# Performance work log

Hardware: AMD Instinct MI355X
Metric: run time of the kernel (lower is better)

Reference implementation:

```python
import jax, jax.numpy as jnp
import numpy as np

E, H, I, G, T, TOPK = 8, 2048, 5632, 128, 256, 2
FP8_MAX = 448.0


def setup_inputs() -> dict:
    key = jax.random.key(0)
    ks = jax.random.split(key, 8)
    hidden_states = jax.random.normal(ks[0], (T, H), jnp.float32)
    router_logits = jax.random.normal(ks[1], (T, E), jnp.float32)
    # unpacked INT4 values in [-8, 7], stored as int8 (modeling unpack_int4->int8)
    w3w1_q = jax.random.randint(ks[2], (E, H, 2 * I), -8, 8, dtype=jnp.int32).astype(jnp.int8)
    w2_q = jax.random.randint(ks[3], (E, I, H), -8, 8, dtype=jnp.int32).astype(jnp.int8)
    # group-wise weight scales: [in_dim/G, out_dim] per expert
    w3w1_scale = jax.random.uniform(ks[4], (E, H // G, 2 * I), jnp.float32, 0.005, 0.02)
    w2_scale = jax.random.uniform(ks[5], (E, I // G, H), jnp.float32, 0.005, 0.02)
    # per-expert static activation scales (p3_p1 = max(p1,p3) pre-folded)
    input_scale_fc1 = jax.random.uniform(ks[6], (E,), jnp.float32, 0.5, 1.5)
    input_scale_fc2 = jax.random.uniform(ks[7], (E,), jnp.float32, 0.5, 1.5)
    return dict(hidden_states=hidden_states, router_logits=router_logits,
                w3w1_q=w3w1_q, w2_q=w2_q, w3w1_scale=w3w1_scale, w2_scale=w2_scale,
                input_scale_fc1=input_scale_fc1, input_scale_fc2=input_scale_fc2)


def _fp8_qdq(x, s):
    # quantize activation to fp8_e4m3 (clamp + round-to-fp8) then dequantize
    q = jnp.clip(x / s, -FP8_MAX, FP8_MAX).astype(jnp.float8_e4m3fn)
    return q.astype(jnp.float32)


def _dequant(w_q, w_scale):
    # w_q: [in, out] int8; w_scale: [in/G, out] -> repeat each group G rows
    return w_q.astype(jnp.float32) * jnp.repeat(w_scale, G, axis=0)


def _routing(router_logits):
    probs = jax.nn.softmax(router_logits, axis=-1)            # [T, E]
    vals, idx = jax.lax.top_k(probs, TOPK)                    # [T, K]
    scales = vals / jnp.sum(vals, axis=-1, keepdims=True)     # renormalize
    # per-token gate weight for every expert, zero if not selected: [T, E]
    gate = jnp.sum(jax.nn.one_hot(idx, E, dtype=scales.dtype) * scales[..., None], axis=1)
    return gate


def reference(hidden_states, router_logits, w3w1_q, w2_q, w3w1_scale, w2_scale,
              input_scale_fc1, input_scale_fc2):
    gate = _routing(router_logits)                            # [T, E]
    out = jnp.zeros_like(hidden_states)
    for e in range(E):  # fixed small expert loop (structurally distinct weights)
        s1 = input_scale_fc1[e]
        act = _fp8_qdq(hidden_states, s1)                     # [T, H]
        w_fc1 = _dequant(w3w1_q[e], w3w1_scale[e])            # [H, 2I]
        fc1 = (act @ w_fc1) * s1                              # [T, 2I]
        up, gt = fc1[:, :I], fc1[:, I:]                       # chunk: (w3 | w1)
        h = up * jax.nn.silu(gt)                              # [T, I]
        s2 = input_scale_fc2[e]
        act2 = _fp8_qdq(h, s2)
        w_fc2 = _dequant(w2_q[e], w2_scale[e])                # [I, H]
        fc2 = (act2 @ w_fc2) * s2                             # [T, H]
        out = out + fc2 * gate[:, e:e + 1]
    return out
```

## Files before the change

kernel.cpp:

```cpp
#include <hip/hip_runtime.h>
#include <hip/hip_bf16.h>
#include <hip/hip_fp8.h>
#include <cstdint>
#include <cstddef>

#define E_ 8
#define H_ 2048
#define I_ 5632
#define N1_ (2 * I_)
#define G_ 128
#define T_ 256
#define RPE 256
#define SLOTS (E_ * RPE)

typedef __attribute__((ext_vector_type(4))) float f32x4;
typedef __attribute__((ext_vector_type(8))) __bf16 bf16x8;

#define WS_CNT 0
#define WS_TOKEN 64
#define WS_GATE (64 + SLOTS * 4)
#define WS_A1 32768
#define WS_A2 (WS_A1 + SLOTS * H_ * 2)

__device__ __forceinline__ uint32_t pack_bf16x2(float a, float b) {
  union { float f; uint32_t u; } ua, ub;
  ua.f = a; ub.f = b;
  uint32_t ra = (ua.u + 0x7FFFu + ((ua.u >> 16) & 1u)) >> 16;
  uint32_t rb = (ub.u + 0x7FFFu + ((ub.u >> 16) & 1u)) & 0xFFFF0000u;
  return ra | rb;
}

__device__ __forceinline__ float fp8_qdq1(float x) {
  x = fminf(fmaxf(x, -448.0f), 448.0f);
  __hip_fp8_e4m3 q(x);
  return (float)q;
}

__global__ void routing_kernel(const float* __restrict__ logits,
                               int* __restrict__ cnt,
                               int* __restrict__ token_of, float* __restrict__ gate_of) {
  __shared__ int s_cnt[E_];
  int t = threadIdx.x;
  if (t < E_) s_cnt[t] = 0;
  __syncthreads();
  float l[E_];
#pragma unroll
  for (int e = 0; e < E_; e++) l[e] = logits[t * E_ + e];
  int i0 = 0;
#pragma unroll
  for (int e = 1; e < E_; e++) if (l[e] > l[i0]) i0 = e;
  int i1 = (i0 == 0) ? 1 : 0;
#pragma unroll
  for (int e = 0; e < E_; e++) if (e != i0 && l[e] > l[i1]) i1 = e;
  float g0 = 1.0f / (1.0f + expf(l[i1] - l[i0]));
  float g1 = 1.0f - g0;
  int s0 = atomicAdd(&s_cnt[i0], 1);
  int s1 = atomicAdd(&s_cnt[i1], 1);
  token_of[i0 * RPE + s0] = t;  gate_of[i0 * RPE + s0] = g0;
  token_of[i1 * RPE + s1] = t;  gate_of[i1 * RPE + s1] = g1;
  __syncthreads();
  if (t < E_) cnt[t] = s_cnt[t];
  for (int idx = t; idx < SLOTS; idx += 256) {
    int e = idx >> 8, r = idx & (RPE - 1);
    if (r >= s_cnt[e]) { token_of[idx] = 0; gate_of[idx] = 0.0f; }
  }
}

__global__ void gather_kernel(const float* __restrict__ hidden,
                              const float* __restrict__ is1,
                              const int* __restrict__ cnt,
                              const int* __restrict__ token_of,
                              __hip_bfloat16* __restrict__ A1) {
  int sg = blockIdx.x;
  int e = sg >> 8, r = sg & (RPE - 1);
  bool pad = (r >= cnt[e]);
  uint4 u;
  if (pad) {
    u.x = u.y = u.z = u.w = 0u;
  } else {
    int t = token_of[sg];
    float s1 = is1[e];
    const float4* hp = (const float4*)(hidden + (size_t)t * H_ + threadIdx.x * 8);
    float4 x0 = hp[0], x1 = hp[1];
    float q0 = fp8_qdq1(x0.x / s1), q1 = fp8_qdq1(x0.y / s1);
    float q2 = fp8_qdq1(x0.z / s1), q3 = fp8_qdq1(x0.w / s1);
    float q4 = fp8_qdq1(x1.x / s1), q5 = fp8_qdq1(x1.y / s1);
    float q6 = fp8_qdq1(x1.z / s1), q7 = fp8_qdq1(x1.w / s1);
    u.x = pack_bf16x2(q0, q1); u.y = pack_bf16x2(q2, q3);
    u.z = pack_bf16x2(q4, q5); u.w = pack_bf16x2(q6, q7);
  }
  ((uint4*)(A1 + (size_t)sg * H_))[threadIdx.x] = u;
}

__global__ __launch_bounds__(256) void fc1_kernel(
    const int* __restrict__ w1, const float* __restrict__ w1s,
    const float* __restrict__ is1v, const float* __restrict__ is2v,
    const __hip_bfloat16* __restrict__ A1, __hip_bfloat16* __restrict__ A2) {
  __shared__ __hip_bfloat16 Bt[2][4][64][8];
  const int e = blockIdx.y;
  const int j0 = blockIdx.x * 32;
  const int tid = threadIdx.x;
  const int wave = tid >> 6, lane = tid & 63;
  const int lm = lane & 15, kq = lane >> 4;
  const int sn = lane;
  const int kb4 = wave * 4;
  const int gcol = (sn < 32) ? (j0 + sn) : (I_ + j0 + (sn - 32));
  const int* wp = w1 + (size_t)e * H_ * N1_ + gcol;
  const float* sbase = w1s + (size_t)e * (H_ / G_) * N1_ + gcol;
  const __hip_bfloat16* abase = A1 + (size_t)e * RPE * H_;

  f32x4 acc[4][4];
#pragma unroll
  for (int a = 0; a < 4; a++)
#pragma unroll
    for (int b = 0; b < 4; b++) acc[a][b] = (f32x4){0.f, 0.f, 0.f, 0.f};

  int wA[8], wB[8];
  float scA = sbase[0], scB = scA;
#pragma unroll
  for (int g = 0; g < 2; g++)
#pragma unroll
    for (int c = 0; c < 4; c++)
      wA[g * 4 + c] = __builtin_nontemporal_load(wp + (size_t)(kb4 + 16 * g + c) * N1_);
#pragma unroll
  for (int g = 0; g < 2; g++) {
    uint32_t p0 = pack_bf16x2((float)wA[g * 4 + 0] * scA, (float)wA[g * 4 + 1] * scA);
    uint32_t p1 = pack_bf16x2((float)wA[g * 4 + 2] * scA, (float)wA[g * 4 + 3] * scA);
    *(uint2*)&Bt[0][(wave >> 1) + 2 * g][sn][(wave & 1) * 4] = make_uint2(p0, p1);
  }
  wp += (size_t)32 * N1_;
#pragma unroll
  for (int g = 0; g < 2; g++)
#pragma unroll
    for (int c = 0; c < 4; c++)
      wB[g * 4 + c] = __builtin_nontemporal_load(wp + (size_t)(kb4 + 16 * g + c) * N1_);
  wp += (size_t)32 * N1_;

  const __hip_bfloat16* aptr[4];
#pragma unroll
  for (int mj = 0; mj < 4; mj++)
    aptr[mj] = abase + (size_t)((wave * 4 + mj) * 16 + lm) * H_ + kq * 8;
  uint4 afr[4];
#pragma unroll
  for (int mj = 0; mj < 4; mj++) afr[mj] = *(const uint4*)aptr[mj];

  __syncthreads();

  for (int ks = 0; ks < 64; ks++) {
    const int buf = ks & 1;
    int wC[8]; float scC = scB;
    if (ks + 2 < 64) {
      if (((ks + 2) & 3) == 0) scC = sbase[(size_t)((ks + 2) >> 2) * N1_];
#pragma unroll
      for (int g = 0; g < 2; g++)
#pragma unroll
        for (int c = 0; c < 4; c++)
          wC[g * 4 + c] = __builtin_nontemporal_load(wp + (size_t)(kb4 + 16 * g + c) * N1_);
    }
    uint4 anx[4];
    if (ks + 1 < 64) {
#pragma unroll
      for (int mj = 0; mj < 4; mj++)
        anx[mj] = *(const uint4*)(aptr[mj] + (ks + 1) * 32);
    }
#pragma unroll
    for (int f = 0; f < 4; f++) {
      union { uint4 u; bf16x8 v; } bu;
      bu.u = *(const uint4*)&Bt[buf][kq][f * 16 + lm][0];
#pragma unroll
      for (int mj = 0; mj < 4; mj++) {
        union { uint4 u; bf16x8 v; } au;
        au.u = afr[mj];
        acc[mj][f] = __builtin_amdgcn_mfma_f32_16x16x32_bf16(au.v, bu.v, acc[mj][f], 0, 0, 0);
      }
    }
    if (ks + 1 < 64) {
#pragma unroll
      for (int g = 0; g < 2; g++) {
        uint32_t p0 = pack_bf16x2((float)wB[g * 4 + 0] * scB, (float)wB[g * 4 + 1] * scB);
        uint32_t p1 = pack_bf16x2((float)wB[g * 4 + 2] * scB, (float)wB[g * 4 + 3] * scB);
        *(uint2*)&Bt[buf ^ 1][(wave >> 1) + 2 * g][sn][(wave & 1) * 4] = make_uint2(p0, p1);
      }
    }
    __syncthreads();
#pragma unroll
    for (int i = 0; i < 8; i++) wB[i] = wC[i];
    scB = scC;
#pragma unroll
    for (int mj = 0; mj < 4; mj++) afr[mj] = anx[mj];
    wp += (size_t)32 * N1_;
  }

  const float s1 = is1v[e], s2 = is2v[e];
  __hip_bfloat16* a2base = A2 + (size_t)(e * RPE) * I_ + j0;
#pragma unroll
  for (int mj = 0; mj < 4; mj++) {
    int mrow = (wave * 4 + mj) * 16 + kq * 4;
#pragma unroll
    for (int r = 0; r < 4; r++) {
#pragma unroll
      for (int f = 0; f < 2; f++) {
        float up = acc[mj][f][r] * s1;
        float gt = acc[mj][f + 2][r] * s1;
        float h = up * (gt / (1.0f + expf(-gt)));
        float q = fp8_qdq1(h / s2);
        a2base[(size_t)(mrow + r) * I_ + f * 16 + lm] = __float2bfloat16(q);
      }
    }
  }
}

__global__ __launch_bounds__(256) void fc2_kernel(
    const int* __restrict__ w2, const float* __restrict__ w2s,
    const float* __restrict__ is2v, const int* __restrict__ cnt,
    const int* __restrict__ token_of, const float* __restrict__ gate_of,
    const __hip_bfloat16* __restrict__ A2, float* __restrict__ out) {
  __shared__ __hip_bfloat16 Bt[2][4][64][8];
  const int e = blockIdx.y;
  const int n0 = blockIdx.x * 64;
  const int z = blockIdx.z;
  const int tid = threadIdx.x;
  const int wave = tid >> 6, lane = tid & 63;
  const int lm = lane & 15, kq = lane >> 4;
  const int sn = lane;
  const int kb4 = wave * 4;
  const int gcol = n0 + sn;
  const int* wp = w2 + (size_t)e * I_ * H_ + (size_t)(z * 44 * 32) * H_ + gcol;
  const float* sbase = w2s + (size_t)e * (I_ / G_) * H_ + gcol;
  const __hip_bfloat16* abase = A2 + (size_t)e * RPE * I_;

  f32x4 acc[4][4];
#pragma unroll
  for (int a = 0; a < 4; a++)
#pragma unroll
    for (int b = 0; b < 4; b++) acc[a][b] = (f32x4){0.f, 0.f, 0.f, 0.f};

  int wA[8], wB[8];
  float scA = sbase[(size_t)(z * 11) * H_], scB = scA;
#pragma unroll
  for (int g = 0; g < 2; g++)
#pragma unroll
    for (int c = 0; c < 4; c++)
      wA[g * 4 + c] = __builtin_nontemporal_load(wp + (size_t)(kb4 + 16 * g + c) * H_);
#pragma unroll
  for (int g = 0; g < 2; g++) {
    uint32_t p0 = pack_bf16x2((float)wA[g * 4 + 0] * scA, (float)wA[g * 4 + 1] * scA);
    uint32_t p1 = pack_bf16x2((float)wA[g * 4 + 2] * scA, (float)wA[g * 4 + 3] * scA);
    *(uint2*)&Bt[0][(wave >> 1) + 2 * g][sn][(wave & 1) * 4] = make_uint2(p0, p1);
  }
  wp += (size_t)32 * H_;
#pragma unroll
  for (int g = 0; g < 2; g++)
#pragma unroll
    for (int c = 0; c < 4; c++)
      wB[g * 4 + c] = __builtin_nontemporal_load(wp + (size_t)(kb4 + 16 * g + c) * H_);
  wp += (size_t)32 * H_;

  const __hip_bfloat16* aptr[4];
#pragma unroll
  for (int mj = 0; mj < 4; mj++)
    aptr[mj] = abase + (size_t)((wave * 4 + mj) * 16 + lm) * I_ + (size_t)z * 44 * 32 + kq * 8;
  uint4 afr[4];
#pragma unroll
  for (int mj = 0; mj < 4; mj++) afr[mj] = *(const uint4*)aptr[mj];

  __syncthreads();

  for (int ks = 0; ks < 44; ks++) {
    const int buf = ks & 1;
    int wC[8]; float scC = scB;
    if (ks + 2 < 44) {
      if (((ks + 2) & 3) == 0) scC = sbase[(size_t)(z * 11 + ((ks + 2) >> 2)) * H_];
#pragma unroll
      for (int g = 0; g < 2; g++)
#pragma unroll
        for (int c = 0; c < 4; c++)
          wC[g * 4 + c] = __builtin_nontemporal_load(wp + (size_t)(kb4 + 16 * g + c) * H_);
    }
    uint4 anx[4];
    if (ks + 1 < 44) {
#pragma unroll
      for (int mj = 0; mj < 4; mj++)
        anx[mj] = *(const uint4*)(aptr[mj] + (ks + 1) * 32);
    }
#pragma unroll
    for (int f = 0; f < 4; f++) {
      union { uint4 u; bf16x8 v; } bu;
      bu.u = *(const uint4*)&Bt[buf][kq][f * 16 + lm][0];
#pragma unroll
      for (int mj = 0; mj < 4; mj++) {
        union { uint4 u; bf16x8 v; } au;
        au.u = afr[mj];
        acc[mj][f] = __builtin_amdgcn_mfma_f32_16x16x32_bf16(au.v, bu.v, acc[mj][f], 0, 0, 0);
      }
    }
    if (ks + 1 < 44) {
#pragma unroll
      for (int g = 0; g < 2; g++) {
        uint32_t p0 = pack_bf16x2((float)wB[g * 4 + 0] * scB, (float)wB[g * 4 + 1] * scB);
        uint32_t p1 = pack_bf16x2((float)wB[g * 4 + 2] * scB, (float)wB[g * 4 + 3] * scB);
        *(uint2*)&Bt[buf ^ 1][(wave >> 1) + 2 * g][sn][(wave & 1) * 4] = make_uint2(p0, p1);
      }
    }
    __syncthreads();
#pragma unroll
    for (int i = 0; i < 8; i++) wB[i] = wC[i];
    scB = scC;
#pragma unroll
    for (int mj = 0; mj < 4; mj++) afr[mj] = anx[mj];
    wp += (size_t)32 * H_;
  }

  const float s2 = is2v[e];
  const int c_n = cnt[e];
#pragma unroll
  for (int mj = 0; mj < 4; mj++) {
    int sl0 = (wave * 4 + mj) * 16 + kq * 4;
#pragma unroll
    for (int r = 0; r < 4; r++) {
      int slot = sl0 + r;
      if (slot < c_n) {
        int t = token_of[e * RPE + slot];
        float gv = gate_of[e * RPE + slot] * s2;
#pragma unroll
        for (int f = 0; f < 4; f++)
          atomicAdd(out + (size_t)t * H_ + n0 + f * 16 + lm, acc[mj][f][r] * gv);
      }
    }
  }
}

extern "C" void kernel_launch(void* const* d_in, const int* in_sizes, int n_in,
                              void* d_out, int out_size, void* d_ws, size_t ws_size,
                              hipStream_t stream) {
  const float* hidden = (const float*)d_in[0];
  const float* logits = (const float*)d_in[1];
  const int* w1 = (const int*)d_in[2];
  const int* w2 = (const int*)d_in[3];
  const float* w1s = (const float*)d_in[4];
  const float* w2s = (const float*)d_in[5];
  const float* is1 = (const float*)d_in[6];
  const float* is2 = (const float*)d_in[7];
  float* out = (float*)d_out;
  char* ws = (char*)d_ws;
  int* cnt = (int*)(ws + WS_CNT);
  int* token_of = (int*)(ws + WS_TOKEN);
  float* gate_of = (float*)(ws + WS_GATE);
  __hip_bfloat16* A1 = (__hip_bfloat16*)(ws + WS_A1);
  __hip_bfloat16* A2 = (__hip_bfloat16*)(ws + WS_A2);

  hipMemsetAsync(d_out, 0, (size_t)T_ * H_ * sizeof(float), stream);
  routing_kernel<<<1, 256, 0, stream>>>(logits, cnt, token_of, gate_of);
  gather_kernel<<<SLOTS, 256, 0, stream>>>(hidden, is1, cnt, token_of, A1);
  fc1_kernel<<<dim3(I_ / 32, E_), 256, 0, stream>>>(w1, w1s, is1, is2, A1, A2);
  fc2_kernel<<<dim3(H_ / 64, E_, 4), 256, 0, stream>>>(w2, w2s, is2, cnt, token_of,
                                                       gate_of, A2, out);
}
```

Before: 1.379 ms.

## Skip MFMA work on empty expert row tiles and use non-draining barriers

Reads each expert's routed-token count in the fc1 and fc2 kernels and computes how many 16-row tiles per wave hold real tokens. Loads, MFMAs and epilogue stores are skipped for inactive tiles, and tiles are interleaved across waves (mj*4+wave) so the active work is spread evenly. The __syncthreads calls are replaced by a barrier that waits only on LDS counters, so outstanding global weight prefetches are not drained each step. The kernels remain bound by streaming the weights, so skipping compute may help little, and the custom barrier relies on the in-flight global loads never being needed before their own wait.

```diff
diff --git a/kernel.cpp b/kernel.cpp
--- a/kernel.cpp
+++ b/kernel.cpp
@@ -34,6 +34,13 @@
   x = fminf(fmaxf(x, -448.0f), 448.0f);
   __hip_fp8_e4m3 q(x);
   return (float)q;
+}
+
+__device__ __forceinline__ void block_sync_nodrain() {
+  __builtin_amdgcn_sched_barrier(0);
+  asm volatile("s_waitcnt lgkmcnt(0)" ::: "memory");
+  __builtin_amdgcn_s_barrier();
+  __builtin_amdgcn_sched_barrier(0);
 }
 
 __global__ void routing_kernel(const float* __restrict__ logits,
@@ -95,6 +102,7 @@
 __global__ __launch_bounds__(256) void fc1_kernel(
     const int* __restrict__ w1, const float* __restrict__ w1s,
     const float* __restrict__ is1v, const float* __restrict__ is2v,
+    const int* __restrict__ cnt,
     const __hip_bfloat16* __restrict__ A1, __hip_bfloat16* __restrict__ A2) {
   __shared__ __hip_bfloat16 Bt[2][4][64][8];
   const int e = blockIdx.y;
@@ -109,6 +117,10 @@
   const float* sbase = w1s + (size_t)e * (H_ / G_) * N1_ + gcol;
   const __hip_bfloat16* abase = A1 + (size_t)e * RPE * H_;
 
+  const int C16 = (cnt[e] + 15) >> 4;
+  int nact = (C16 - wave + 3) >> 2;
+  if (nact < 0) nact = 0;
+
   f32x4 acc[4][4];
 #pragma unroll
   for (int a = 0; a < 4; a++)
@@ -137,14 +149,14 @@
   wp += (size_t)32 * N1_;
 
   const __hip_bfloat16* aptr[4];
-#pragma unroll
-  for (int mj = 0; mj < 4; mj++)
-    aptr[mj] = abase + (size_t)((wave * 4 + mj) * 16 + lm) * H_ + kq * 8;
   uint4 afr[4];
 #pragma unroll
-  for (int mj = 0; mj < 4; mj++) afr[mj] = *(const uint4*)aptr[mj];
-
-  __syncthreads();
+  for (int mj = 0; mj < 4; mj++) {
+    aptr[mj] = abase + (size_t)((mj * 4 + wave) * 16 + lm) * H_ + kq * 8;
+    if (mj < nact) afr[mj] = *(const uint4*)aptr[mj];
+  }
+
+  block_sync_nodrain();
 
   for (int ks = 0; ks < 64; ks++) {
     const int buf = ks & 1;
@@ -161,17 +173,33 @@
     if (ks + 1 < 64) {
 #pragma unroll
       for (int mj = 0; mj < 4; mj++)
-        anx[mj] = *(const uint4*)(aptr[mj] + (ks + 1) * 32);
-    }
-#pragma unroll
-    for (int f = 0; f < 4; f++) {
-      union { uint4 u; bf16x8 v; } bu;
-      bu.u = *(const uint4*)&Bt[buf][kq][f * 16 + lm][0];
-#pragma unroll
-      for (int mj = 0; mj < 4; mj++) {
-        union { uint4 u; bf16x8 v; } au;
-        au.u = afr[mj];
-        acc[mj][f] = __builtin_amdgcn_mfma_f32_16x16x32_bf16(au.v, bu.v, acc[mj][f], 0, 0, 0);
+        if (mj < nact) anx[mj] = *(const uint4*)(aptr[mj] + (ks + 1) * 32);
+    }
+    if (nact == 4) {
+#pragma unroll
+      for (int f = 0; f < 4; f++) {
+        union { uint4 u; bf16x8 v; } bu;
+        bu.u = *(const uint4*)&Bt[buf][kq][f * 16 + lm][0];
+#pragma unroll
+        for (int mj = 0; mj < 4; mj++) {
+          union { uint4 u; bf16x8 v; } au;
+          au.u = afr[mj];
+          acc[mj][f] = __builtin_amdgcn_mfma_f32_16x16x32_bf16(au.v, bu.v, acc[mj][f], 0, 0, 0);
+        }
+      }
+    } else if (nact > 0) {
+#pragma unroll
+      for (int f = 0; f < 4; f++) {
+        union { uint4 u; bf16x8 v; } bu;
+        bu.u = *(const uint4*)&Bt[buf][kq][f * 16 + lm][0];
+#pragma unroll
+        for (int mj = 0; mj < 4; mj++) {
+          if (mj < nact) {
+            union { uint4 u; bf16x8 v; } au;
+            au.u = afr[mj];
+            acc[mj][f] = __builtin_amdgcn_mfma_f32_16x16x32_bf16(au.v, bu.v, acc[mj][f], 0, 0, 0);
+          }
+        }
       }
     }
     if (ks + 1 < 64) {
@@ -182,7 +210,7 @@
         *(uint2*)&Bt[buf ^ 1][(wave >> 1) + 2 * g][sn][(wave & 1) * 4] = make_uint2(p0, p1);
       }
     }
-    __syncthreads();
+    block_sync_nodrain();
 #pragma unroll
     for (int i = 0; i < 8; i++) wB[i] = wC[i];
     scB = scC;
@@ -195,16 +223,18 @@
   __hip_bfloat16* a2base = A2 + (size_t)(e * RPE) * I_ + j0;
 #pragma unroll
   for (int mj = 0; mj < 4; mj++) {
-    int mrow = (wave * 4 + mj) * 16 + kq * 4;
-#pragma unroll
-    for (int r = 0; r < 4; r++) {
-#pragma unroll
-      for (int f = 0; f < 2; f++) {
-        float up = acc[mj][f][r] * s1;
-        float gt = acc[mj][f + 2][r] * s1;
-        float h = up * (gt / (1.0f + expf(-gt)));
-        float q = fp8_qdq1(h / s2);
-        a2base[(size_t)(mrow + r) * I_ + f * 16 + lm] = __float2bfloat16(q);
+    if (mj < nact) {
+      int mrow = (mj * 4 + wave) * 16 + kq * 4;
+#pragma unroll
+      for (int r = 0; r < 4; r++) {
+#pragma unroll
+        for (int f = 0; f < 2; f++) {
+          float up = acc[mj][f][r] * s1;
+          float gt = acc[mj][f + 2][r] * s1;
+          float h = up * (gt / (1.0f + expf(-gt)));
+          float q = fp8_qdq1(h / s2);
+          a2base[(size_t)(mrow + r) * I_ + f * 16 + lm] = __float2bfloat16(q);
+        }
       }
     }
   }
@@ -229,6 +259,11 @@
   const float* sbase = w2s + (size_t)e * (I_ / G_) * H_ + gcol;
   const __hip_bfloat16* abase = A2 + (size_t)e * RPE * I_;
 
+  const int c_n = cnt[e];
+  const int C16 = (c_n + 15) >> 4;
+  int nact = (C16 - wave + 3) >> 2;
+  if (nact < 0) nact = 0;
+
   f32x4 acc[4][4];
 #pragma unroll
   for (int a = 0; a < 4; a++)
@@ -257,14 +292,14 @@
   wp += (size_t)32 * H_;
 
   const __hip_bfloat16* aptr[4];
-#pragma unroll
-  for (int mj = 0; mj < 4; mj++)
-    aptr[mj] = abase + (size_t)((wave * 4 + mj) * 16 + lm) * I_ + (size_t)z * 44 * 32 + kq * 8;
   uint4 afr[4];
 #pragma unroll
-  for (int mj = 0; mj < 4; mj++) afr[mj] = *(const uint4*)aptr[mj];
-
-  __syncthreads();
+  for (int mj = 0; mj < 4; mj++) {
+    aptr[mj] = abase + (size_t)((mj * 4 + wave) * 16 + lm) * I_ + (size_t)z * 44 * 32 + kq * 8;
+    if (mj < nact) afr[mj] = *(const uint4*)aptr[mj];
+  }
+
+  block_sync_nodrain();
 
   for (int ks = 0; ks < 44; ks++) {
     const int buf = ks & 1;
@@ -281,17 +316,33 @@
     if (ks + 1 < 44) {
 #pragma unroll
       for (int mj = 0; mj < 4; mj++)
-        anx[mj] = *(const uint4*)(aptr[mj] + (ks + 1) * 32);
-    }
-#pragma unroll
-    for (int f = 0; f < 4; f++) {
-      union { uint4 u; bf16x8 v; } bu;
-      bu.u = *(const uint4*)&Bt[buf][kq][f * 16 + lm][0];
-#pragma unroll
-      for (int mj = 0; mj < 4; mj++) {
-        union { uint4 u; bf16x8 v; } au;
-        au.u = afr[mj];
-        acc[mj][f] = __builtin_amdgcn_mfma_f32_16x16x32_bf16(au.v, bu.v, acc[mj][f], 0, 0, 0);
+        if (mj < nact) anx[mj] = *(const uint4*)(aptr[mj] + (ks + 1) * 32);
+    }
+    if (nact == 4) {
+#pragma unroll
+      for (int f = 0; f < 4; f++) {
+        union { uint4 u; bf16x8 v; } bu;
+        bu.u = *(const uint4*)&Bt[buf][kq][f * 16 + lm][0];
+#pragma unroll
+        for (int mj = 0; mj < 4; mj++) {
+          union { uint4 u; bf16x8 v; } au;
+          au.u = afr[mj];
+          acc[mj][f] = __builtin_amdgcn_mfma_f32_16x16x32_bf16(au.v, bu.v, acc[mj][f], 0, 0, 0);
+        }
+      }
+    } else if (nact > 0) {
+#pragma unroll
+      for (int f = 0; f < 4; f++) {
+        union { uint4 u; bf16x8 v; } bu;
+        bu.u = *(const uint4*)&Bt[buf][kq][f * 16 + lm][0];
+#pragma unroll
+        for (int mj = 0; mj < 4; mj++) {
+          if (mj < nact) {
+            union { uint4 u; bf16x8 v; } au;
+            au.u = afr[mj];
+            acc[mj][f] = __builtin_amdgcn_mfma_f32_16x16x32_bf16(au.v, bu.v, acc[mj][f], 0, 0, 0);
+          }
+        }
       }
     }
     if (ks + 1 < 44) {
@@ -302,7 +353,7 @@
         *(uint2*)&Bt[buf ^ 1][(wave >> 1) + 2 * g][sn][(wave & 1) * 4] = make_uint2(p0, p1);
       }
     }
-    __syncthreads();
+    block_sync_nodrain();
 #pragma unroll
     for (int i = 0; i < 8; i++) wB[i] = wC[i];
     scB = scC;
@@ -312,19 +363,20 @@
   }
 
   const float s2 = is2v[e];
-  const int c_n = cnt[e];
 #pragma unroll
   for (int mj = 0; mj < 4; mj++) {
-    int sl0 = (wave * 4 + mj) * 16 + kq * 4;
-#pragma unroll
-    for (int r = 0; r < 4; r++) {
-      int slot = sl0 + r;
-      if (slot < c_n) {
-        int t = token_of[e * RPE + slot];
-        float gv = gate_of[e * RPE + slot] * s2;
-#pragma unroll
-        for (int f = 0; f < 4; f++)
-          atomicAdd(out + (size_t)t * H_ + n0 + f * 16 + lm, acc[mj][f][r] * gv);
+    if (mj < nact) {
+      int sl0 = (mj * 4 + wave) * 16 + kq * 4;
+#pragma unroll
+      for (int r = 0; r < 4; r++) {
+        int slot = sl0 + r;
+        if (slot < c_n) {
+          int t = token_of[e * RPE + slot];
+          float gv = gate_of[e * RPE + slot] * s2;
+#pragma unroll
+          for (int f = 0; f < 4; f++)
+            atomicAdd(out + (size_t)t * H_ + n0 + f * 16 + lm, acc[mj][f][r] * gv);
+        }
       }
     }
   }
@@ -352,7 +404,7 @@
   hipMemsetAsync(d_out, 0, (size_t)T_ * H_ * sizeof(float), stream);
   routing_kernel<<<1, 256, 0, stream>>>(logits, cnt, token_of, gate_of);
   gather_kernel<<<SLOTS, 256, 0, stream>>>(hidden, is1, cnt, token_of, A1);
-  fc1_kernel<<<dim3(I_ / 32, E_), 256, 0, stream>>>(w1, w1s, is1, is2, A1, A2);
+  fc1_kernel<<<dim3(I_ / 32, E_), 256, 0, stream>>>(w1, w1s, is1, is2, cnt, A1, A2);
   fc2_kernel<<<dim3(H_ / 64, E_, 4), 256, 0, stream>>>(w2, w2s, is2, cnt, token_of,
                                                        gate_of, A2, out);
 }
```

After: 1.277 ms. 1.08x faster.

## Skip empty expert row tiles and restructure weight pipeline with non-draining barriers

Applied to the files above, without the earlier changes.

Both GEMM kernels now read each expert's token count and run MFMAs, A loads and epilogue stores only for the 16-row tiles that hold routed tokens. The row tiles are interleaved across waves so the active work is spread evenly. Weight loads become 2-wide int vector loads with per-pair scale loads, and the k loop is unrolled by two with explicit register double buffers. A custom barrier waits only on LDS counters, so in-flight global loads are not drained at each sync. This mainly cuts wasted MFMA work, since about 64 of 256 slots per expert are used on average, but it adds more manual scheduling and relies on the asm waitcnt being correct.

```diff
diff --git a/kernel.cpp b/kernel.cpp
--- a/kernel.cpp
+++ b/kernel.cpp
@@ -15,6 +15,7 @@
 
 typedef __attribute__((ext_vector_type(4))) float f32x4;
 typedef __attribute__((ext_vector_type(8))) __bf16 bf16x8;
+typedef __attribute__((ext_vector_type(2))) int i32x2;
 
 #define WS_CNT 0
 #define WS_TOKEN 64
@@ -34,6 +35,54 @@
   x = fminf(fmaxf(x, -448.0f), 448.0f);
   __hip_fp8_e4m3 q(x);
   return (float)q;
+}
+
+__device__ __forceinline__ void block_sync_nodrain() {
+  __builtin_amdgcn_sched_barrier(0);
+  asm volatile("s_waitcnt lgkmcnt(0)" ::: "memory");
+  __builtin_amdgcn_s_barrier();
+  __builtin_amdgcn_sched_barrier(0);
+}
+
+__device__ __forceinline__ void wissue(const int* __restrict__ wpt, size_t ldN, int m,
+                                       i32x2 wv[4]) {
+#pragma unroll
+  for (int c = 0; c < 4; ++c)
+    wv[c] = __builtin_nontemporal_load(
+        reinterpret_cast<const i32x2*>(wpt + ((size_t)m * 32 + c) * ldN));
+}
+
+__device__ __forceinline__ void wstage(__hip_bfloat16 (*Btb)[64][8], int kqw, int n0, int h4,
+                                       const i32x2 wv[4], float2 sc) {
+  uint32_t a0 = pack_bf16x2((float)wv[0].x * sc.x, (float)wv[1].x * sc.x);
+  uint32_t a1 = pack_bf16x2((float)wv[2].x * sc.x, (float)wv[3].x * sc.x);
+  uint32_t b0 = pack_bf16x2((float)wv[0].y * sc.y, (float)wv[1].y * sc.y);
+  uint32_t b1 = pack_bf16x2((float)wv[2].y * sc.y, (float)wv[3].y * sc.y);
+  *(uint2*)&Btb[kqw][n0][h4] = make_uint2(a0, a1);
+  *(uint2*)&Btb[kqw][n0 + 1][h4] = make_uint2(b0, b1);
+}
+
+__device__ __forceinline__ void aissue(const __hip_bfloat16* const aptr[4], int m, int nact,
+                                       uint4 av[4]) {
+#pragma unroll
+  for (int mj = 0; mj < 4; ++mj)
+    if (mj < nact) av[mj] = *(const uint4*)(aptr[mj] + (size_t)m * 32);
+}
+
+__device__ __forceinline__ void do_mfma(const __hip_bfloat16 (*Btb)[64][8], int kq, int lm,
+                                        int nact, const uint4 afr[4], f32x4 acc[4][4]) {
+#pragma unroll
+  for (int f = 0; f < 4; ++f) {
+    union { uint4 u; bf16x8 v; } bu;
+    bu.u = *(const uint4*)&Btb[kq][f * 16 + lm][0];
+#pragma unroll
+    for (int mj = 0; mj < 4; ++mj)
+      if (mj < nact) {
+        union { uint4 u; bf16x8 v; } au;
+        au.u = afr[mj];
+        acc[mj][f] = __builtin_amdgcn_mfma_f32_16x16x32_bf16(au.v, bu.v, acc[mj][f], 0, 0, 0);
+      }
+  }
 }
 
 __global__ void routing_kernel(const float* __restrict__ logits,
@@ -95,6 +144,7 @@
 __global__ __launch_bounds__(256) void fc1_kernel(
     const int* __restrict__ w1, const float* __restrict__ w1s,
     const float* __restrict__ is1v, const float* __restrict__ is2v,
+    const int* __restrict__ cnt,
     const __hip_bfloat16* __restrict__ A1, __hip_bfloat16* __restrict__ A2) {
   __shared__ __hip_bfloat16 Bt[2][4][64][8];
   const int e = blockIdx.y;
@@ -102,109 +152,76 @@
   const int tid = threadIdx.x;
   const int wave = tid >> 6, lane = tid & 63;
   const int lm = lane & 15, kq = lane >> 4;
-  const int sn = lane;
-  const int kb4 = wave * 4;
-  const int gcol = (sn < 32) ? (j0 + sn) : (I_ + j0 + (sn - 32));
-  const int* wp = w1 + (size_t)e * H_ * N1_ + gcol;
-  const float* sbase = w1s + (size_t)e * (H_ / G_) * N1_ + gcol;
+  const int np = tid & 31, kg = tid >> 5;
+  const int kqw = kg >> 1, h4 = (kg & 1) * 4;
+  const int n0s = np * 2;
+  const int gc2 = (n0s < 32) ? (j0 + n0s) : (I_ + j0 + (n0s - 32));
+  const int* wpt = w1 + (size_t)e * H_ * N1_ + (size_t)(kg * 4) * N1_ + gc2;
+  const float* spt = w1s + (size_t)e * (H_ / G_) * N1_ + gc2;
   const __hip_bfloat16* abase = A1 + (size_t)e * RPE * H_;
 
+  const int C16 = (cnt[e] + 15) >> 4;
+  int nact = (C16 - wave + 3) >> 2;
+  if (nact < 0) nact = 0;
+
   f32x4 acc[4][4];
 #pragma unroll
   for (int a = 0; a < 4; a++)
 #pragma unroll
     for (int b = 0; b < 4; b++) acc[a][b] = (f32x4){0.f, 0.f, 0.f, 0.f};
 
-  int wA[8], wB[8];
-  float scA = sbase[0], scB = scA;
-#pragma unroll
-  for (int g = 0; g < 2; g++)
-#pragma unroll
-    for (int c = 0; c < 4; c++)
-      wA[g * 4 + c] = __builtin_nontemporal_load(wp + (size_t)(kb4 + 16 * g + c) * N1_);
-#pragma unroll
-  for (int g = 0; g < 2; g++) {
-    uint32_t p0 = pack_bf16x2((float)wA[g * 4 + 0] * scA, (float)wA[g * 4 + 1] * scA);
-    uint32_t p1 = pack_bf16x2((float)wA[g * 4 + 2] * scA, (float)wA[g * 4 + 3] * scA);
-    *(uint2*)&Bt[0][(wave >> 1) + 2 * g][sn][(wave & 1) * 4] = make_uint2(p0, p1);
-  }
-  wp += (size_t)32 * N1_;
-#pragma unroll
-  for (int g = 0; g < 2; g++)
-#pragma unroll
-    for (int c = 0; c < 4; c++)
-      wB[g * 4 + c] = __builtin_nontemporal_load(wp + (size_t)(kb4 + 16 * g + c) * N1_);
-  wp += (size_t)32 * N1_;
-
   const __hip_bfloat16* aptr[4];
 #pragma unroll
   for (int mj = 0; mj < 4; mj++)
-    aptr[mj] = abase + (size_t)((wave * 4 + mj) * 16 + lm) * H_ + kq * 8;
-  uint4 afr[4];
-#pragma unroll
-  for (int mj = 0; mj < 4; mj++) afr[mj] = *(const uint4*)aptr[mj];
-
-  __syncthreads();
-
-  for (int ks = 0; ks < 64; ks++) {
-    const int buf = ks & 1;
-    int wC[8]; float scC = scB;
-    if (ks + 2 < 64) {
-      if (((ks + 2) & 3) == 0) scC = sbase[(size_t)((ks + 2) >> 2) * N1_];
-#pragma unroll
-      for (int g = 0; g < 2; g++)
-#pragma unroll
-        for (int c = 0; c < 4; c++)
-          wC[g * 4 + c] = __builtin_nontemporal_load(wp + (size_t)(kb4 + 16 * g + c) * N1_);
-    }
-    uint4 anx[4];
-    if (ks + 1 < 64) {
-#pragma unroll
-      for (int mj = 0; mj < 4; mj++)
-        anx[mj] = *(const uint4*)(aptr[mj] + (ks + 1) * 32);
-    }
-#pragma unroll
-    for (int f = 0; f < 4; f++) {
-      union { uint4 u; bf16x8 v; } bu;
-      bu.u = *(const uint4*)&Bt[buf][kq][f * 16 + lm][0];
-#pragma unroll
-      for (int mj = 0; mj < 4; mj++) {
-        union { uint4 u; bf16x8 v; } au;
-        au.u = afr[mj];
-        acc[mj][f] = __builtin_amdgcn_mfma_f32_16x16x32_bf16(au.v, bu.v, acc[mj][f], 0, 0, 0);
-      }
-    }
-    if (ks + 1 < 64) {
-#pragma unroll
-      for (int g = 0; g < 2; g++) {
-        uint32_t p0 = pack_bf16x2((float)wB[g * 4 + 0] * scB, (float)wB[g * 4 + 1] * scB);
-        uint32_t p1 = pack_bf16x2((float)wB[g * 4 + 2] * scB, (float)wB[g * 4 + 3] * scB);
-        *(uint2*)&Bt[buf ^ 1][(wave >> 1) + 2 * g][sn][(wave & 1) * 4] = make_uint2(p0, p1);
-      }
-    }
-    __syncthreads();
-#pragma unroll
-    for (int i = 0; i < 8; i++) wB[i] = wC[i];
-    scB = scC;
-#pragma unroll
-    for (int mj = 0; mj < 4; mj++) afr[mj] = anx[mj];
-    wp += (size_t)32 * N1_;
-  }
+    aptr[mj] = abase + (size_t)((mj * 4 + wave) * 16 + lm) * H_ + kq * 8;
+
+  i32x2 wv0[4], wv1[4];
+  uint4 av0[4], av1[4];
+  float2 sc0 = *(const float2*)spt;
+  float2 sc1 = sc0;
+  wissue(wpt, N1_, 0, wv0);
+  wissue(wpt, N1_, 1, wv1);
+  aissue(aptr, 0, nact, av1);
+  wstage(Bt[0], kqw, n0s, h4, wv0, sc0);
+  block_sync_nodrain();
+
+  for (int i = 0; i < 31; ++i) {
+    const int ks = 2 * i;
+    if (((ks + 2) & 3) == 0) sc0 = *(const float2*)(spt + (size_t)((ks + 2) >> 2) * N1_);
+    wissue(wpt, N1_, ks + 2, wv0);
+    aissue(aptr, ks + 1, nact, av0);
+    do_mfma(Bt[0], kq, lm, nact, av1, acc);
+    wstage(Bt[1], kqw, n0s, h4, wv1, sc1);
+    block_sync_nodrain();
+    if (((ks + 3) & 3) == 1) sc1 = *(const float2*)(spt + (size_t)((ks + 3) >> 2) * N1_);
+    wissue(wpt, N1_, ks + 3, wv1);
+    aissue(aptr, ks + 2, nact, av1);
+    do_mfma(Bt[1], kq, lm, nact, av0, acc);
+    wstage(Bt[0], kqw, n0s, h4, wv0, sc0);
+    block_sync_nodrain();
+  }
+  aissue(aptr, 63, nact, av0);
+  do_mfma(Bt[0], kq, lm, nact, av1, acc);
+  wstage(Bt[1], kqw, n0s, h4, wv1, sc1);
+  block_sync_nodrain();
+  do_mfma(Bt[1], kq, lm, nact, av0, acc);
 
   const float s1 = is1v[e], s2 = is2v[e];
   __hip_bfloat16* a2base = A2 + (size_t)(e * RPE) * I_ + j0;
 #pragma unroll
   for (int mj = 0; mj < 4; mj++) {
-    int mrow = (wave * 4 + mj) * 16 + kq * 4;
-#pragma unroll
-    for (int r = 0; r < 4; r++) {
-#pragma unroll
-      for (int f = 0; f < 2; f++) {
-        float up = acc[mj][f][r] * s1;
-        float gt = acc[mj][f + 2][r] * s1;
-        float h = up * (gt / (1.0f + expf(-gt)));
-        float q = fp8_qdq1(h / s2);
-        a2base[(size_t)(mrow + r) * I_ + f * 16 + lm] = __float2bfloat16(q);
+    if (mj < nact) {
+      int mrow = (mj * 4 + wave) * 16 + kq * 4;
+#pragma unroll
+      for (int r = 0; r < 4; r++) {
+#pragma unroll
+        for (int f = 0; f < 2; f++) {
+          float up = acc[mj][f][r] * s1;
+          float gt = acc[mj][f + 2][r] * s1;
+          float h = up * (gt / (1.0f + expf(-gt)));
+          float q = fp8_qdq1(h / s2);
+          a2base[(size_t)(mrow + r) * I_ + f * 16 + lm] = __float2bfloat16(q);
+        }
       }
     }
   }
@@ -222,109 +239,79 @@
   const int tid = threadIdx.x;
   const int wave = tid >> 6, lane = tid & 63;
   const int lm = lane & 15, kq = lane >> 4;
-  const int sn = lane;
-  const int kb4 = wave * 4;
-  const int gcol = n0 + sn;
-  const int* wp = w2 + (size_t)e * I_ * H_ + (size_t)(z * 44 * 32) * H_ + gcol;
-  const float* sbase = w2s + (size_t)e * (I_ / G_) * H_ + gcol;
+  const int np = tid & 31, kg = tid >> 5;
+  const int kqw = kg >> 1, h4 = (kg & 1) * 4;
+  const int n0s = np * 2;
+  const int gc2 = n0 + n0s;
+  const int z11 = z * 11;
+  const int* wpt = w2 + (size_t)e * I_ * H_ + (size_t)(z * 44 * 32 + kg * 4) * H_ + gc2;
+  const float* spt = w2s + (size_t)e * (I_ / G_) * H_ + gc2;
   const __hip_bfloat16* abase = A2 + (size_t)e * RPE * I_;
 
+  const int c_n = cnt[e];
+  const int C16 = (c_n + 15) >> 4;
+  int nact = (C16 - wave + 3) >> 2;
+  if (nact < 0) nact = 0;
+
   f32x4 acc[4][4];
 #pragma unroll
   for (int a = 0; a < 4; a++)
 #pragma unroll
     for (int b = 0; b < 4; b++) acc[a][b] = (f32x4){0.f, 0.f, 0.f, 0.f};
 
-  int wA[8], wB[8];
-  float scA = sbase[(size_t)(z * 11) * H_], scB = scA;
-#pragma unroll
-  for (int g = 0; g < 2; g++)
-#pragma unroll
-    for (int c = 0; c < 4; c++)
-      wA[g * 4 + c] = __builtin_nontemporal_load(wp + (size_t)(kb4 + 16 * g + c) * H_);
-#pragma unroll
-  for (int g = 0; g < 2; g++) {
-    uint32_t p0 = pack_bf16x2((float)wA[g * 4 + 0] * scA, (float)wA[g * 4 + 1] * scA);
-    uint32_t p1 = pack_bf16x2((float)wA[g * 4 + 2] * scA, (float)wA[g * 4 + 3] * scA);
-    *(uint2*)&Bt[0][(wave >> 1) + 2 * g][sn][(wave & 1) * 4] = make_uint2(p0, p1);
-  }
-  wp += (size_t)32 * H_;
-#pragma unroll
-  for (int g = 0; g < 2; g++)
-#pragma unroll
-    for (int c = 0; c < 4; c++)
-      wB[g * 4 + c] = __builtin_nontemporal_load(wp + (size_t)(kb4 + 16 * g + c) * H_);
-  wp += (size_t)32 * H_;
-
   const __hip_bfloat16* aptr[4];
 #pragma unroll
   for (int mj = 0; mj < 4; mj++)
-    aptr[mj] = abase + (size_t)((wave * 4 + mj) * 16 + lm) * I_ + (size_t)z * 44 * 32 + kq * 8;
-  uint4 afr[4];
-#pragma unroll
-  for (int mj = 0; mj < 4; mj++) afr[mj] = *(const uint4*)aptr[mj];
-
-  __syncthreads();
-
-  for (int ks = 0; ks < 44; ks++) {
-    const int buf = ks & 1;
-    int wC[8]; float scC = scB;
-    if (ks + 2 < 44) {
-      if (((ks + 2) & 3) == 0) scC = sbase[(size_t)(z * 11 + ((ks + 2) >> 2)) * H_];
-#pragma unroll
-      for (int g = 0; g < 2; g++)
-#pragma unroll
-        for (int c = 0; c < 4; c++)
-          wC[g * 4 + c] = __builtin_nontemporal_load(wp + (size_t)(kb4 + 16 * g + c) * H_);
-    }
-    uint4 anx[4];
-    if (ks + 1 < 44) {
-#pragma unroll
-      for (int mj = 0; mj < 4; mj++)
-        anx[mj] = *(const uint4*)(aptr[mj] + (ks + 1) * 32);
-    }
-#pragma unroll
-    for (int f = 0; f < 4; f++) {
-      union { uint4 u; bf16x8 v; } bu;
-      bu.u = *(const uint4*)&Bt[buf][kq][f * 16 + lm][0];
-#pragma unroll
-      for (int mj = 0; mj < 4; mj++) {
-        union { uint4 u; bf16x8 v; } au;
-        au.u = afr[mj];
-        acc[mj][f] = __builtin_amdgcn_mfma_f32_16x16x32_bf16(au.v, bu.v, acc[mj][f], 0, 0, 0);
-      }
-    }
-    if (ks + 1 < 44) {
-#pragma unroll
-      for (int g = 0; g < 2; g++) {
-        uint32_t p0 = pack_bf16x2((float)wB[g * 4 + 0] * scB, (float)wB[g * 4 + 1] * scB);
-        uint32_t p1 = pack_bf16x2((float)wB[g * 4 + 2] * scB, (float)wB[g * 4 + 3] * scB);
-        *(uint2*)&Bt[buf ^ 1][(wave >> 1) + 2 * g][sn][(wave & 1) * 4] = make_uint2(p0, p1);
-      }
-    }
-    __syncthreads();
-#pragma unroll
-    for (int i = 0; i < 8; i++) wB[i] = wC[i];
-    scB = scC;
-#pragma unroll
-    for (int mj = 0; mj < 4; mj++) afr[mj] = anx[mj];
-    wp += (size_t)32 * H_;
-  }
+    aptr[mj] = abase + (size_t)((mj * 4 + wave) * 16 + lm) * I_ + (size_t)z * 44 * 32 + kq * 8;
+
+  i32x2 wv0[4], wv1[4];
+  uint4 av0[4], av1[4];
+  float2 sc0 = *(const float2*)(spt + (size_t)z11 * H_);
+  float2 sc1 = sc0;
+  wissue(wpt, H_, 0, wv0);
+  wissue(wpt, H_, 1, wv1);
+  aissue(aptr, 0, nact, av1);
+  wstage(Bt[0], kqw, n0s, h4, wv0, sc0);
+  block_sync_nodrain();
+
+  for (int i = 0; i < 21; ++i) {
+    const int ks = 2 * i;
+    if (((ks + 2) & 3) == 0)
+      sc0 = *(const float2*)(spt + (size_t)(z11 + ((ks + 2) >> 2)) * H_);
+    wissue(wpt, H_, ks + 2, wv0);
+    aissue(aptr, ks + 1, nact, av0);
+    do_mfma(Bt[0], kq, lm, nact, av1, acc);
+    wstage(Bt[1], kqw, n0s, h4, wv1, sc1);
+    block_sync_nodrain();
+    if (((ks + 3) & 3) == 1)
+      sc1 = *(const float2*)(spt + (size_t)(z11 + ((ks + 3) >> 2)) * H_);
+    wissue(wpt, H_, ks + 3, wv1);
+    aissue(aptr, ks + 2, nact, av1);
+    do_mfma(Bt[1], kq, lm, nact, av0, acc);
+    wstage(Bt[0], kqw, n0s, h4, wv0, sc0);
+    block_sync_nodrain();
+  }
+  aissue(aptr, 43, nact, av0);
+  do_mfma(Bt[0], kq, lm, nact, av1, acc);
+  wstage(Bt[1], kqw, n0s, h4, wv1, sc1);
+  block_sync_nodrain();
+  do_mfma(Bt[1], kq, lm, nact, av0, acc);
 
   const float s2 = is2v[e];
-  const int c_n = cnt[e];
 #pragma unroll
   for (int mj = 0; mj < 4; mj++) {
-    int sl0 = (wave * 4 + mj) * 16 + kq * 4;
-#pragma unroll
-    for (int r = 0; r < 4; r++) {
-      int slot = sl0 + r;
-      if (slot < c_n) {
-        int t = token_of[e * RPE + slot];
-        float gv = gate_of[e * RPE + slot] * s2;
-#pragma unroll
-        for (int f = 0; f < 4; f++)
-          atomicAdd(out + (size_t)t * H_ + n0 + f * 16 + lm, acc[mj][f][r] * gv);
+    if (mj < nact) {
+      int sl0 = (mj * 4 + wave) * 16 + kq * 4;
+#pragma unroll
+      for (int r = 0; r < 4; r++) {
+        int slot = sl0 + r;
+        if (slot < c_n) {
+          int t = token_of[e * RPE + slot];
+          float gv = gate_of[e * RPE + slot] * s2;
+#pragma unroll
+          for (int f = 0; f < 4; f++)
+            atomicAdd(out + (size_t)t * H_ + n0 + f * 16 + lm, acc[mj][f][r] * gv);
+        }
       }
     }
   }
@@ -352,7 +339,7 @@
   hipMemsetAsync(d_out, 0, (size_t)T_ * H_ * sizeof(float), stream);
   routing_kernel<<<1, 256, 0, stream>>>(logits, cnt, token_of, gate_of);
   gather_kernel<<<SLOTS, 256, 0, stream>>>(hidden, is1, cnt, token_of, A1);
-  fc1_kernel<<<dim3(I_ / 32, E_), 256, 0, stream>>>(w1, w1s, is1, is2, A1, A2);
+  fc1_kernel<<<dim3(I_ / 32, E_), 256, 0, stream>>>(w1, w1s, is1, is2, cnt, A1, A2);
   fc2_kernel<<<dim3(H_ / 64, E_, 4), 256, 0, stream>>>(w2, w2s, is2, cnt, token_of,
                                                        gate_of, A2, out);
 }
```

Measured after the change: 1.242 ms. 1.11x faster.
